# Kernel tuning notes

Measured on AMD Instinct MI355X. Metric: run time of the kernel, lower is better.

## Reference

```python
import jax, jax.numpy as jnp
import numpy as np

N_EMBD = 1024
D_FF = 4096
N_EXPERTS = 8
TOP_K = 2


def setup_inputs() -> dict:
    key = jax.random.key(0)
    k1, k2, k3, k4 = jax.random.split(key, 4)
    x = jax.random.normal(k1, (1, 2048, N_EMBD), dtype=jnp.float32)
    mask = jnp.ones((2048, N_EXPERTS), dtype=jnp.float32)
    Wr = jax.random.normal(k2, (N_EMBD, N_EXPERTS), dtype=jnp.float32) * 0.02
    W1 = jax.random.normal(k3, (N_EXPERTS, N_EMBD, D_FF), dtype=jnp.float32) * 0.02
    W2 = jax.random.normal(k4, (N_EXPERTS, D_FF, N_EMBD), dtype=jnp.float32) * 0.02
    return {"x": x, "mask": mask, "Wr": Wr, "W1": W1, "W2": W2}


def reference(x, mask, Wr, W1, W2):
    T = x.shape[0] * x.shape[1]
    xs = x.reshape(T, N_EMBD)                      # [T, d]
    router_logits = (xs @ Wr) * mask               # [T, E], masked as in MaskedMoE
    all_probs = jax.nn.softmax(router_logits, axis=-1)  # softmax_topk order
    weights, selected = jax.lax.top_k(all_probs, TOP_K)  # [T, K]
    # combine[t, e] = sum of routing weights where token t selected expert e
    combine = jnp.zeros((T, N_EXPERTS), dtype=xs.dtype)
    combine = combine.at[jnp.arange(T)[:, None], selected].add(weights)
    results = jnp.zeros_like(xs)
    for e in range(N_EXPERTS):  # fixed small expert count
        h = jax.nn.gelu(xs @ W1[e])                # [T, d_ff]
        out = h @ W2[e]                            # [T, d]
        results = results + combine[:, e:e + 1] * out
    return results.reshape(x.shape)
```

## Files before the change

kernel.cpp:

```cpp
#include <hip/hip_runtime.h>
#include <hip/hip_bf16.h>


#define T_TOK 2048
#define D_EMB 1024
#define DFF   4096
#define NE    8

typedef _Float16 f16x8 __attribute__((ext_vector_type(8)));
typedef float    f32x4 __attribute__((ext_vector_type(4)));

__device__ __forceinline__ float gelu_tanh(float x) {
    const float c = 0.7978845608028654f;
    float z = c * (x + 0.044715f * x * x * x);
    float u = __expf(2.0f * z);
    return 0.5f * x * (1.0f + (u - 1.0f) / (u + 1.0f));
}

__device__ __forceinline__ void gll(const void* g, void* l) {
    __builtin_amdgcn_global_load_lds((__attribute__((address_space(1))) void*)g,
                                     (__attribute__((address_space(3))) void*)l,
                                     16, 0, 0);
}

__global__ void k_zero(int* counts) {
    if (threadIdx.x < NE) counts[threadIdx.x] = 0;
}

__global__ __launch_bounds__(256) void k_router(
    const float* __restrict__ x, const float* __restrict__ mask,
    const float* __restrict__ Wr, _Float16* __restrict__ xh,
    int* __restrict__ counts, int* __restrict__ elist,
    int* __restrict__ tok_e, int* __restrict__ tok_p, float* __restrict__ tok_w) {
    int wave = threadIdx.x >> 6;
    int lane = threadIdx.x & 63;
    int t = blockIdx.x * 4 + wave;
    if (t >= T_TOK) return;

    float acc[NE];
#pragma unroll
    for (int e = 0; e < NE; e++) acc[e] = 0.f;
    const float* xr = x + (size_t)t * D_EMB;
    for (int c = 0; c < D_EMB / 64; c++) {
        int i = c * 64 + lane;
        float xv = xr[i];
        xh[(size_t)t * D_EMB + i] = (_Float16)xv;
        const float* wr = Wr + (size_t)i * NE;
#pragma unroll
        for (int e = 0; e < NE; e++) acc[e] += xv * wr[e];
    }
#pragma unroll
    for (int e = 0; e < NE; e++) {
#pragma unroll
        for (int off = 32; off > 0; off >>= 1)
            acc[e] += __shfl_xor(acc[e], off);
    }
    if (lane == 0) {
        float p[NE];
        float mx = -1e30f;
#pragma unroll
        for (int e = 0; e < NE; e++) {
            p[e] = acc[e] * mask[t * NE + e];
            mx = fmaxf(mx, p[e]);
        }
        float s = 0.f;
#pragma unroll
        for (int e = 0; e < NE; e++) { p[e] = expf(p[e] - mx); s += p[e]; }
#pragma unroll
        for (int e = 0; e < NE; e++) p[e] /= s;
        int e0 = 0; float b0 = p[0];
#pragma unroll
        for (int e = 1; e < NE; e++) if (p[e] > b0) { b0 = p[e]; e0 = e; }
        int e1 = -1; float b1 = -1.f;
#pragma unroll
        for (int e = 0; e < NE; e++) if (e != e0 && p[e] > b1) { b1 = p[e]; e1 = e; }

        int pos0 = atomicAdd(&counts[e0], 1);
        elist[e0 * T_TOK + pos0] = t;
        tok_e[t * 2 + 0] = e0; tok_p[t * 2 + 0] = pos0; tok_w[t * 2 + 0] = b0;
        int pos1 = atomicAdd(&counts[e1], 1);
        elist[e1 * T_TOK + pos1] = t;
        tok_e[t * 2 + 1] = e1; tok_p[t * 2 + 1] = pos1; tok_w[t * 2 + 1] = b1;
    }
}

__global__ __launch_bounds__(256) void k_transpose(
    const float* __restrict__ W1, const float* __restrict__ W2,
    _Float16* __restrict__ W1T, _Float16* __restrict__ W2T) {
    __shared__ float tile[64][65];
    int bz = blockIdx.z;
    int e = bz & 7;
    bool isW2 = bz >= 8;
    const float* S = (isW2 ? W2 : W1) + (size_t)e * 4194304;
    _Float16* D = (isW2 ? W2T : W1T) + (size_t)e * 4194304;
    int src_ld = isW2 ? 1024 : 4096;
    int dst_ld = isW2 ? 4096 : 1024;
    int bx = blockIdx.x;
    int nb, kb;
    if (isW2) { nb = (bx & 15) * 64; kb = (bx >> 4) * 64; }
    else      { nb = (bx & 63) * 64; kb = (bx >> 6) * 64; }
    int t = threadIdx.x;
#pragma unroll
    for (int i = 0; i < 4; i++) {
        int r = (t >> 4) + i * 16;
        int c = (t & 15) * 4;
        float4 v = *(const float4*)(S + (size_t)(kb + r) * src_ld + nb + c);
        tile[r][c + 0] = v.x; tile[r][c + 1] = v.y;
        tile[r][c + 2] = v.z; tile[r][c + 3] = v.w;
    }
    __syncthreads();
#pragma unroll
    for (int j = 0; j < 2; j++) {
        int idx = j * 256 + t;
        int n = idx >> 3, kc = idx & 7;
        f16x8 o;
#pragma unroll
        for (int u = 0; u < 8; u++) o[u] = (_Float16)tile[kc * 8 + u][n];
        *(f16x8*)(D + (size_t)(nb + n) * dst_ld + kb + kc * 8) = o;
    }
}


__global__ __launch_bounds__(256) void k_gemm1(
    const _Float16* __restrict__ xh, const _Float16* __restrict__ BT,
    const int* __restrict__ counts, const int* __restrict__ elist,
    _Float16* __restrict__ H) {
    int e = blockIdx.z;
    int cnt = counts[e];
    int p0 = blockIdx.y * 128;
    if (p0 >= cnt) return;
    int rowbase = 0;
    for (int i = 0; i < NE; i++) rowbase += (i < e) ? counts[i] : 0;
    int n0 = blockIdx.x * 128;
    const _Float16* B = BT + (size_t)e * 4194304;

    __shared__ _Float16 As[128 * 64];
    __shared__ _Float16 Bs[128 * 64];
    __shared__ int ttok[128];

    int tid = threadIdx.x;
    if (tid < 128) ttok[tid] = elist[e * T_TOK + min(p0 + tid, cnt - 1)];
    __syncthreads();

    int w = tid >> 6, lane = tid & 63;
    int rq = tid >> 3;
    int cch = (tid & 7) ^ ((tid >> 3) & 7);
    const _Float16* pA[4];
    const _Float16* pB[4];
    _Float16* lA[4];
    _Float16* lB[4];
#pragma unroll
    for (int q = 0; q < 4; q++) {
        int row = q * 32 + rq;
        pA[q] = xh + (size_t)ttok[row] * D_EMB + cch * 8;
        pB[q] = B + (size_t)(n0 + row) * 1024 + cch * 8;
        lA[q] = As + (q * 256 + w * 64) * 8;
        lB[q] = Bs + (q * 256 + w * 64) * 8;
    }

    int wm = w >> 1, wn = w & 1;
    int lhi = lane >> 4, llo = lane & 15;
    int m7 = llo & 7;
    int kc0 = lhi ^ m7, kc1 = kc0 ^ 4;
    const _Float16* arp0 = As + (wm * 64 + llo) * 64 + kc0 * 8;
    const _Float16* arp1 = As + (wm * 64 + llo) * 64 + kc1 * 8;
    const _Float16* brp0 = Bs + (wn * 64 + llo) * 64 + kc0 * 8;
    const _Float16* brp1 = Bs + (wn * 64 + llo) * 64 + kc1 * 8;

    f32x4 acc[4][4] = {};
    for (int it = 0; it < 16; ++it) {
        __syncthreads();
#pragma unroll
        for (int q = 0; q < 4; q++) { gll(pA[q], lA[q]); gll(pB[q], lB[q]); }
#pragma unroll
        for (int q = 0; q < 4; q++) { pA[q] += 64; pB[q] += 64; }
        __syncthreads();
        f16x8 a[4], b[4];
#pragma unroll
        for (int i = 0; i < 4; i++) {
            a[i] = *(const f16x8*)(arp0 + i * 1024);
            b[i] = *(const f16x8*)(brp0 + i * 1024);
        }
#pragma unroll
        for (int mt = 0; mt < 4; mt++)
#pragma unroll
            for (int nt = 0; nt < 4; nt++)
                acc[mt][nt] = __builtin_amdgcn_mfma_f32_16x16x32_f16(a[mt], b[nt], acc[mt][nt], 0, 0, 0);
#pragma unroll
        for (int i = 0; i < 4; i++) {
            a[i] = *(const f16x8*)(arp1 + i * 1024);
            b[i] = *(const f16x8*)(brp1 + i * 1024);
        }
#pragma unroll
        for (int mt = 0; mt < 4; mt++)
#pragma unroll
            for (int nt = 0; nt < 4; nt++)
                acc[mt][nt] = __builtin_amdgcn_mfma_f32_16x16x32_f16(a[mt], b[nt], acc[mt][nt], 0, 0, 0);
    }

#pragma unroll
    for (int mt = 0; mt < 4; mt++) {
#pragma unroll
        for (int i = 0; i < 4; i++) {
            int p = p0 + wm * 64 + mt * 16 + lhi * 4 + i;
            if (p < cnt) {
                size_t rowoff = (size_t)(rowbase + p) * DFF + n0 + wn * 64 + llo;
#pragma unroll
                for (int nt = 0; nt < 4; nt++)
                    H[rowoff + nt * 16] = (_Float16)gelu_tanh(acc[mt][nt][i]);
            }
        }
    }
}

__global__ __launch_bounds__(256) void k_gemm2(
    const _Float16* __restrict__ H, const _Float16* __restrict__ BT,
    const int* __restrict__ counts, float* __restrict__ Obase) {
    int bz = blockIdx.z;
    int e = bz & 7, sp = bz >> 3;
    int cnt = counts[e];
    int p0 = blockIdx.y * 128;
    if (p0 >= cnt) return;
    int rowbase = 0;
    for (int i = 0; i < NE; i++) rowbase += (i < e) ? counts[i] : 0;
    int n0 = blockIdx.x * 128;
    int kh = sp * 1024;
    const _Float16* B = BT + (size_t)e * 4194304;
    float* O = Obase + (size_t)sp * 4194304;

    __shared__ _Float16 As[128 * 64];
    __shared__ _Float16 Bs[128 * 64];

    int tid = threadIdx.x;
    int w = tid >> 6, lane = tid & 63;
    int rq = tid >> 3;
    int cch = (tid & 7) ^ ((tid >> 3) & 7);
    const _Float16* pA[4];
    const _Float16* pB[4];
    _Float16* lA[4];
    _Float16* lB[4];
#pragma unroll
    for (int q = 0; q < 4; q++) {
        int row = q * 32 + rq;
        int r = rowbase + min(p0 + row, cnt - 1);
        pA[q] = H + (size_t)r * DFF + kh + cch * 8;
        pB[q] = B + (size_t)(n0 + row) * 4096 + kh + cch * 8;
        lA[q] = As + (q * 256 + w * 64) * 8;
        lB[q] = Bs + (q * 256 + w * 64) * 8;
    }

    int wm = w >> 1, wn = w & 1;
    int lhi = lane >> 4, llo = lane & 15;
    int m7 = llo & 7;
    int kc0 = lhi ^ m7, kc1 = kc0 ^ 4;
    const _Float16* arp0 = As + (wm * 64 + llo) * 64 + kc0 * 8;
    const _Float16* arp1 = As + (wm * 64 + llo) * 64 + kc1 * 8;
    const _Float16* brp0 = Bs + (wn * 64 + llo) * 64 + kc0 * 8;
    const _Float16* brp1 = Bs + (wn * 64 + llo) * 64 + kc1 * 8;

    f32x4 acc[4][4] = {};
    for (int it = 0; it < 16; ++it) {
        __syncthreads();
#pragma unroll
        for (int q = 0; q < 4; q++) { gll(pA[q], lA[q]); gll(pB[q], lB[q]); }
#pragma unroll
        for (int q = 0; q < 4; q++) { pA[q] += 64; pB[q] += 64; }
        __syncthreads();
        f16x8 a[4], b[4];
#pragma unroll
        for (int i = 0; i < 4; i++) {
            a[i] = *(const f16x8*)(arp0 + i * 1024);
            b[i] = *(const f16x8*)(brp0 + i * 1024);
        }
#pragma unroll
        for (int mt = 0; mt < 4; mt++)
#pragma unroll
            for (int nt = 0; nt < 4; nt++)
                acc[mt][nt] = __builtin_amdgcn_mfma_f32_16x16x32_f16(a[mt], b[nt], acc[mt][nt], 0, 0, 0);
#pragma unroll
        for (int i = 0; i < 4; i++) {
            a[i] = *(const f16x8*)(arp1 + i * 1024);
            b[i] = *(const f16x8*)(brp1 + i * 1024);
        }
#pragma unroll
        for (int mt = 0; mt < 4; mt++)
#pragma unroll
            for (int nt = 0; nt < 4; nt++)
                acc[mt][nt] = __builtin_amdgcn_mfma_f32_16x16x32_f16(a[mt], b[nt], acc[mt][nt], 0, 0, 0);
    }

#pragma unroll
    for (int mt = 0; mt < 4; mt++) {
#pragma unroll
        for (int i = 0; i < 4; i++) {
            int p = p0 + wm * 64 + mt * 16 + lhi * 4 + i;
            if (p < cnt) {
                size_t o = (size_t)(rowbase + p) * D_EMB + n0 + wn * 64 + llo;
#pragma unroll
                for (int nt = 0; nt < 4; nt++)
                    O[o + nt * 16] = acc[mt][nt][i];
            }
        }
    }
}

__global__ __launch_bounds__(256) void k_final(
    const float* __restrict__ Obase, const int* __restrict__ counts,
    const int* __restrict__ tok_e, const int* __restrict__ tok_p,
    const float* __restrict__ tok_w, float* __restrict__ out) {
    __shared__ int sb[NE];
    int t = blockIdx.x;
    if (threadIdx.x == 0) {
        int s = 0;
        for (int e = 0; e < NE; e++) { sb[e] = s; s += counts[e]; }
    }
    __syncthreads();
    int r0 = sb[tok_e[t * 2 + 0]] + tok_p[t * 2 + 0];
    int r1 = sb[tok_e[t * 2 + 1]] + tok_p[t * 2 + 1];
    float w0 = tok_w[t * 2 + 0], w1 = tok_w[t * 2 + 1];
    int i = threadIdx.x * 4;
    float4 s0 = {0, 0, 0, 0}, s1 = {0, 0, 0, 0};
#pragma unroll
    for (int sp = 0; sp < 4; sp++) {
        const float* O = Obase + (size_t)sp * 4194304;
        float4 a = *(const float4*)(O + (size_t)r0 * D_EMB + i);
        float4 b = *(const float4*)(O + (size_t)r1 * D_EMB + i);
        s0.x += a.x; s0.y += a.y; s0.z += a.z; s0.w += a.w;
        s1.x += b.x; s1.y += b.y; s1.z += b.z; s1.w += b.w;
    }
    float4 o;
    o.x = w0 * s0.x + w1 * s1.x;
    o.y = w0 * s0.y + w1 * s1.y;
    o.z = w0 * s0.z + w1 * s1.z;
    o.w = w0 * s0.w + w1 * s1.w;
    *(float4*)(out + (size_t)t * D_EMB + i) = o;
}

extern "C" void kernel_launch(void* const* d_in, const int* in_sizes, int n_in,
                              void* d_out, int out_size, void* d_ws, size_t ws_size,
                              hipStream_t stream) {
    const float* x    = (const float*)d_in[0];
    const float* mask = (const float*)d_in[1];
    const float* Wr   = (const float*)d_in[2];
    const float* W1   = (const float*)d_in[3];
    const float* W2   = (const float*)d_in[4];
    float* out = (float*)d_out;

    char* ws = (char*)d_ws;
    const size_t MB = 1024 * 1024;
    int*      counts = (int*)(ws + 0);
    int*      elist  = (int*)(ws + 1024);
    int*      tok_e  = (int*)(ws + 1024 + 65536);
    int*      tok_p  = (int*)(ws + 1024 + 65536 + 16384);
    float*    tok_w  = (float*)(ws + 1024 + 65536 + 32768);
    _Float16* xh     = (_Float16*)(ws + 1 * MB);
    _Float16* W1T    = (_Float16*)(ws + 8 * MB);
    _Float16* W2T    = (_Float16*)(ws + 72 * MB);
    _Float16* H      = (_Float16*)(ws + 136 * MB);
    float*    Obuf   = (float*)(ws + 168 * MB);

    k_zero<<<1, 64, 0, stream>>>(counts);
    k_router<<<T_TOK / 4, 256, 0, stream>>>(x, mask, Wr, xh, counts, elist, tok_e, tok_p, tok_w);
    k_transpose<<<dim3(1024, 1, 16), 256, 0, stream>>>(W1, W2, W1T, W2T);
    k_gemm1<<<dim3(32, 16, NE), 256, 0, stream>>>(xh, W1T, counts, elist, H);
    k_gemm2<<<dim3(8, 16, 32), 256, 0, stream>>>(H, W2T, counts, Obuf);
    k_final<<<T_TOK, 256, 0, stream>>>(Obuf, counts, tok_e, tok_p, tok_w, out);
}
```

Baseline: 506.8 us.

## Store transposed weights in pre-swizzled K-tiled planes for contiguous GEMM loads

```diff
diff --git a/kernel.cpp b/kernel.cpp
--- a/kernel.cpp
+++ b/kernel.cpp
@@ -87,36 +87,46 @@
 __global__ __launch_bounds__(256) void k_transpose(
     const float* __restrict__ W1, const float* __restrict__ W2,
     _Float16* __restrict__ W1T, _Float16* __restrict__ W2T) {
-    __shared__ float tile[64][65];
+    __shared__ float tile[64 * 132];
     int bz = blockIdx.z;
     int e = bz & 7;
     bool isW2 = bz >= 8;
     const float* S = (isW2 ? W2 : W1) + (size_t)e * 4194304;
-    _Float16* D = (isW2 ? W2T : W1T) + (size_t)e * 4194304;
-    int src_ld = isW2 ? 1024 : 4096;
-    int dst_ld = isW2 ? 4096 : 1024;
+    _Float16* Dst = (isW2 ? W2T : W1T) + (size_t)e * 4194304;
+    int src_ld   = isW2 ? 1024 : 4096;
+    int plane_sz = isW2 ? 65536 : 262144;
     int bx = blockIdx.x;
-    int nb, kb;
-    if (isW2) { nb = (bx & 15) * 64; kb = (bx >> 4) * 64; }
-    else      { nb = (bx & 63) * 64; kb = (bx >> 6) * 64; }
-    int t = threadIdx.x;
+    int kt, nb;
+    if (isW2) { kt = bx >> 3; nb = (bx & 7) * 128; }
+    else      { kt = bx >> 5; nb = (bx & 31) * 128; }
+    int kb = kt * 64;
+    int tid = threadIdx.x;
+
+#pragma unroll
+    for (int i = 0; i < 8; i++) {
+        int f = i * 256 + tid;
+        int row = f >> 5;
+        int col4 = f & 31;
+        float4 v = *(const float4*)(S + (size_t)(kb + row) * src_ld + nb + col4 * 4);
+        int col4s = col4 ^ ((row >> 3) & 7);
+        *(float4*)(&tile[row * 132 + col4s * 4]) = v;
+    }
+    __syncthreads();
+
+    _Float16* plane = Dst + (size_t)kt * plane_sz;
 #pragma unroll
     for (int i = 0; i < 4; i++) {
-        int r = (t >> 4) + i * 16;
-        int c = (t & 15) * 4;
-        float4 v = *(const float4*)(S + (size_t)(kb + r) * src_ld + nb + c);
-        tile[r][c + 0] = v.x; tile[r][c + 1] = v.y;
-        tile[r][c + 2] = v.z; tile[r][c + 3] = v.w;
-    }
-    __syncthreads();
-#pragma unroll
-    for (int j = 0; j < 2; j++) {
-        int idx = j * 256 + t;
-        int n = idx >> 3, kc = idx & 7;
+        int idx = i * 256 + tid;
+        int n = idx >> 3;
+        int c = idx & 7;
         f16x8 o;
 #pragma unroll
-        for (int u = 0; u < 8; u++) o[u] = (_Float16)tile[kc * 8 + u][n];
-        *(f16x8*)(D + (size_t)(nb + n) * dst_ld + kb + kc * 8) = o;
+        for (int u = 0; u < 8; u++) {
+            int k = c * 8 + u;
+            int col4s = (n >> 2) ^ ((k >> 3) & 7);
+            o[u] = (_Float16)tile[k * 132 + col4s * 4 + (n & 3)];
+        }
+        *(f16x8*)(plane + (size_t)(nb + n) * 64 + (c ^ (n & 7)) * 8) = o;
     }
 }
 
@@ -153,7 +163,7 @@
     for (int q = 0; q < 4; q++) {
         int row = q * 32 + rq;
         pA[q] = xh + (size_t)ttok[row] * D_EMB + cch * 8;
-        pB[q] = B + (size_t)(n0 + row) * 1024 + cch * 8;
+        pB[q] = B + (size_t)n0 * 64 + (q * 256 + tid) * 8;
         lA[q] = As + (q * 256 + w * 64) * 8;
         lB[q] = Bs + (q * 256 + w * 64) * 8;
     }
@@ -173,7 +183,7 @@
 #pragma unroll
         for (int q = 0; q < 4; q++) { gll(pA[q], lA[q]); gll(pB[q], lB[q]); }
 #pragma unroll
-        for (int q = 0; q < 4; q++) { pA[q] += 64; pB[q] += 64; }
+        for (int q = 0; q < 4; q++) { pA[q] += 64; pB[q] += 262144; }
         __syncthreads();
         f16x8 a[4], b[4];
 #pragma unroll
@@ -244,7 +254,7 @@
         int row = q * 32 + rq;
         int r = rowbase + min(p0 + row, cnt - 1);
         pA[q] = H + (size_t)r * DFF + kh + cch * 8;
-        pB[q] = B + (size_t)(n0 + row) * 4096 + kh + cch * 8;
+        pB[q] = B + (size_t)(sp * 16) * 65536 + (size_t)n0 * 64 + (q * 256 + tid) * 8;
         lA[q] = As + (q * 256 + w * 64) * 8;
         lB[q] = Bs + (q * 256 + w * 64) * 8;
     }
@@ -264,7 +274,7 @@
 #pragma unroll
         for (int q = 0; q < 4; q++) { gll(pA[q], lA[q]); gll(pB[q], lB[q]); }
 #pragma unroll
-        for (int q = 0; q < 4; q++) { pA[q] += 64; pB[q] += 64; }
+        for (int q = 0; q < 4; q++) { pA[q] += 64; pB[q] += 65536; }
         __syncthreads();
         f16x8 a[4], b[4];
 #pragma unroll
@@ -361,7 +371,7 @@
 
     k_zero<<<1, 64, 0, stream>>>(counts);
     k_router<<<T_TOK / 4, 256, 0, stream>>>(x, mask, Wr, xh, counts, elist, tok_e, tok_p, tok_w);
-    k_transpose<<<dim3(1024, 1, 16), 256, 0, stream>>>(W1, W2, W1T, W2T);
+    k_transpose<<<dim3(512, 1, 16), 256, 0, stream>>>(W1, W2, W1T, W2T);
     k_gemm1<<<dim3(32, 16, NE), 256, 0, stream>>>(xh, W1T, counts, elist, H);
     k_gemm2<<<dim3(8, 16, 32), 256, 0, stream>>>(H, W2T, counts, Obuf);
     k_final<<<T_TOK, 256, 0, stream>>>(Obuf, counts, tok_e, tok_p, tok_w, out);
```

After: 495.8 us. 1.02x faster.
